# Optimization experiments

Measured on AMD Instinct MI355X. Metric: run time of the kernel, lower is better.

## Reference

```python
import jax, jax.numpy as jnp
import numpy as np

B, T, D = 4, 2048, 1024
E = 16            # routed experts
S = 2             # shared experts
MOE_TOPK = 2
COSINE_LAMBDA = 0.1


def setup_inputs() -> dict:
    key = jax.random.key(0)
    k_x, k_g, k_sh, k_rt = jax.random.split(key, 4)
    x = jax.random.normal(k_x, (B, T, D), dtype=jnp.float32)
    gate_w = jax.random.normal(k_g, (E, D), dtype=jnp.float32) * 0.02
    gate_b = jnp.zeros((E,), dtype=jnp.float32)
    shared_experts = jax.random.normal(k_sh, (S, D), dtype=jnp.float32) * 0.1
    routed_experts = jax.random.normal(k_rt, (E, D), dtype=jnp.float32) * 0.1
    return {"x": x, "gate_w": gate_w, "gate_b": gate_b,
            "shared_experts": shared_experts, "routed_experts": routed_experts}


def reference(x, gate_w, gate_b, shared_experts, routed_experts):
    b, t, d = x.shape
    n = b * t
    hidden = x.reshape(n, d)                                   # [N, D]

    # ---- router ----
    logits = hidden @ gate_w.T + gate_b                        # [N, E]
    probs = jax.nn.softmax(logits, axis=-1)                    # stable (shift-invariant)
    topk_vals, topk_idx = jax.lax.top_k(probs, MOE_TOPK)       # [N, K]
    if MOE_TOPK == 1:
        weights = jnp.ones_like(topk_vals)
    else:
        weights = topk_vals / jnp.clip(topk_vals.sum(-1, keepdims=True), 1e-6)

    # ---- shared experts (always active): sum_e hidden * w_e ----
    shared_sum = hidden * shared_experts.sum(0)                # [N, D]

    # ---- dense all-expert elementwise scale (as in original) ----
    routed_outs = hidden[None, :, :] * routed_experts[:, None, :]   # [E, N, D]

    # ---- diversity loss: cosine sim between flattened expert outputs ----
    flat = routed_outs.reshape(E, -1)                          # [E, N*D]
    norms = jnp.maximum(jnp.linalg.norm(flat, axis=1, keepdims=True), 1e-8)
    normed = flat / norms
    sim = jnp.clip(normed @ normed.T, -1.0, 1.0)               # [E, E]
    mask = 1.0 - jnp.eye(E, dtype=sim.dtype)
    div_loss = (sim * mask).sum() / max(E * (E - 1), 1) * COSINE_LAMBDA

    # ---- top-k gather + weighted combine ----
    routed_nd = routed_outs.transpose(1, 0, 2)                 # [N, E, D]
    sel = jnp.take_along_axis(routed_nd, topk_idx[:, :, None], axis=1)  # [N, K, D]
    dyn_sum = (sel * weights[:, :, None]).sum(axis=1)          # [N, D]

    out = (shared_sum + dyn_sum).reshape(b, t, d)
    return out, div_loss
```

## Files before the change

### kernel.cpp

```cpp
#include <hip/hip_runtime.h>

#define NTOK 8192
#define DDIM 1024
#define NEXP 16
#define NPAIR 136
#define NREP 8
#define XROW 1032

typedef float vfloat4 __attribute__((ext_vector_type(4)));

#define WS_GWT 0
#define WS_SG  16384
#define WS_GP  (16384 + NREP * DDIM)
#define WS_RT  (16384 + NREP * DDIM + 16 * NPAIR)

__global__ __launch_bounds__(256) void moe_prep(
    const float* __restrict__ gate_w,
    float* __restrict__ ws)
{
    const int gid = blockIdx.x * 256 + threadIdx.x;
    const int e = gid & 15;
    const int d4 = gid >> 4;
    const float4* gw4 = (const float4*)gate_w;
    float4* gwT4 = (float4*)(ws + WS_GWT);
    gwT4[d4 * 16 + e] = gw4[e * 256 + d4];
    float* s_glob = ws + WS_SG;
    s_glob[gid] = 0.f;
    s_glob[gid + 4096] = 0.f;
}

__global__ __launch_bounds__(256, 4) void moe_route(
    const float* __restrict__ x,
    const float* __restrict__ gate_b,
    float* __restrict__ ws)
{
    __shared__ float xt[8][XROW];

    const int t = threadIdx.x;
    const int b = blockIdx.x;
    const float4* gwT4 = (const float4*)(ws + WS_GWT);
    float* s_glob = ws + WS_SG;
    float4* route = (float4*)(ws + WS_RT);

    float4 ss = make_float4(0.f, 0.f, 0.f, 0.f);
    {
        const float4* x4 = (const float4*)x + (size_t)b * 2048;
        #pragma unroll
        for (int i = 0; i < 8; ++i) {
            float4 v = x4[i * 256 + t];
            *(float4*)&xt[i][4 * t] = v;
            ss.x = fmaf(v.x, v.x, ss.x);
            ss.y = fmaf(v.y, v.y, ss.y);
            ss.z = fmaf(v.z, v.z, ss.z);
            ss.w = fmaf(v.w, v.w, ss.w);
        }
    }
    __syncthreads();

    const int lane = t & 63;
    const int wave = t >> 6;
    const int e = lane & 15;
    const int h = (lane >> 4) & 1;
    const int g = lane >> 5;

    const int tokL = wave * 2 + g;
    const float* xrow = &xt[tokL][h * 512];
    const float4* gt = gwT4 + h * 128 * 16;
    float4 a4 = make_float4(0.f, 0.f, 0.f, 0.f);
    #pragma unroll 8
    for (int i = 0; i < 128; ++i) {
        float4 xv = *(const float4*)(xrow + 4 * i);
        float4 gv = gt[i * 16 + e];
        a4.x = fmaf(xv.x, gv.x, a4.x);
        a4.y = fmaf(xv.y, gv.y, a4.y);
        a4.z = fmaf(xv.z, gv.z, a4.z);
        a4.w = fmaf(xv.w, gv.w, a4.w);
    }
    float acc = (a4.x + a4.y) + (a4.z + a4.w);
    acc += __shfl_xor(acc, 16, 64);
    acc += gate_b[e];

    float v0 = -3.0e38f, v1 = -3.0e38f;
    int i0 = 0, i1 = 0;
    const int base = lane & 32;
    #pragma unroll
    for (int j = 0; j < NEXP; ++j) {
        float lv = __shfl(acc, base + j, 64);
        if (lv > v0)      { v1 = v0; i1 = i0; v0 = lv; i0 = j; }
        else if (lv > v1) { v1 = lv; i1 = j; }
    }
    float ex = __expf(v1 - v0);
    float w0 = 1.f / (1.f + ex);
    float w1 = ex * w0;

    if ((lane & 31) == 0)
        route[b * 8 + tokL] =
            make_float4(w0, w1, __int_as_float(i0), __int_as_float(i1));

    {
        float* rep = s_glob + (size_t)(b & (NREP - 1)) * DDIM;
        atomicAdd(&rep[4 * t + 0], ss.x);
        atomicAdd(&rep[4 * t + 1], ss.y);
        atomicAdd(&rep[4 * t + 2], ss.z);
        atomicAdd(&rep[4 * t + 3], ss.w);
    }
}

__global__ __launch_bounds__(256, 8) void moe_combine(
    const float* __restrict__ x,
    const float* __restrict__ sh,
    const float* __restrict__ re,
    const float* __restrict__ ws,
    float* __restrict__ out)
{
    const int t = threadIdx.x;
    const int lane = t & 63;
    const int n = blockIdx.x * 4 + (t >> 6);
    const float4* route = (const float4*)(ws + WS_RT);

    float4 rec = route[n];
    const float a0 = rec.x, a1 = rec.y;
    const int e0 = __float_as_int(rec.z);
    const int e1 = __float_as_int(rec.w);

    const float4* s0 = (const float4*)sh;
    const float4* s1 = (const float4*)(sh + DDIM);
    const float4* xr = (const float4*)(x + (size_t)n * DDIM);
    const float4* r0 = (const float4*)(re + (size_t)e0 * DDIM);
    const float4* r1 = (const float4*)(re + (size_t)e1 * DDIM);
    vfloat4* o = (vfloat4*)(out + (size_t)n * DDIM);

    #pragma unroll
    for (int j = 0; j < 4; ++j) {
        const int idx = lane + 64 * j;
        float4 xv = xr[idx];
        float4 p  = s0[idx];
        float4 q  = s1[idx];
        float4 b0 = r0[idx];
        float4 b1 = r1[idx];
        vfloat4 r;
        r.x = xv.x * ((p.x + q.x) + a0 * b0.x + a1 * b1.x);
        r.y = xv.y * ((p.y + q.y) + a0 * b0.y + a1 * b1.y);
        r.z = xv.z * ((p.z + q.z) + a0 * b0.z + a1 * b1.z);
        r.w = xv.w * ((p.w + q.w) + a0 * b0.w + a1 * b1.w);
        __builtin_nontemporal_store(r, &o[idx]);
    }
}

__global__ __launch_bounds__(320) void moe_div_partial(
    const float* __restrict__ re,
    float* __restrict__ ws)
{
    __shared__ float reT[64][17];
    __shared__ float s4[4][64];
    __shared__ float s_loc[64];

    const int t = threadIdx.x;
    const int b = blockIdx.x;
    const int d0 = b * 64;
    const float* s_glob = ws + WS_SG;
    float* G_part = ws + WS_GP;

    if (t < 256) {
        int c = t & 63, r = t >> 6;
        s4[r][c] = s_glob[r * DDIM + d0 + c] + s_glob[(r + 4) * DDIM + d0 + c];
        int e = t >> 4, d4 = t & 15;
        float4 v = ((const float4*)(re + (size_t)e * DDIM + d0))[d4];
        reT[d4 * 4 + 0][e] = v.x;
        reT[d4 * 4 + 1][e] = v.y;
        reT[d4 * 4 + 2][e] = v.z;
        reT[d4 * 4 + 3][e] = v.w;
    }
    __syncthreads();
    if (t < 64) s_loc[t] = (s4[0][t] + s4[1][t]) + (s4[2][t] + s4[3][t]);
    __syncthreads();

    const int p = t >> 1;
    const int half = t & 1;
    float a = 0.f;
    if (p < NPAIR) {
        int pe = 0, rem = p;
        while (rem >= NEXP - pe) { rem -= NEXP - pe; ++pe; }
        int pf = pe + rem;
        #pragma unroll
        for (int i = 0; i < 32; ++i) {
            int dd = half * 32 + i;
            a += s_loc[dd] * reT[dd][pe] * reT[dd][pf];
        }
    }
    a += __shfl_down(a, 1, 64);
    if (p < NPAIR && half == 0) G_part[b * NPAIR + p] = a;
}

__global__ __launch_bounds__(192) void moe_div_final(
    const float* __restrict__ ws,
    float* __restrict__ div_out)
{
    __shared__ float G[NPAIR];
    __shared__ float nr[NEXP];
    __shared__ float lsum;
    const float* G_part = ws + WS_GP;
    const int t = threadIdx.x;

    if (t == 0) lsum = 0.f;
    if (t < NPAIR) {
        float g = 0.f;
        #pragma unroll
        for (int b = 0; b < 16; ++b) g += G_part[b * NPAIR + t];
        G[t] = g;
    }
    __syncthreads();
    if (t < NEXP) {
        int idx = t * NEXP - (t * (t - 1)) / 2;
        nr[t] = fmaxf(sqrtf(G[idx]), 1e-8f);
    }
    __syncthreads();
    if (t < NPAIR) {
        int pe = 0, rem = t;
        while (rem >= NEXP - pe) { rem -= NEXP - pe; ++pe; }
        int pf = pe + rem;
        if (pe != pf) {
            float sim = G[t] / (nr[pe] * nr[pf]);
            sim = fminf(1.f, fmaxf(-1.f, sim));
            atomicAdd(&lsum, 2.f * sim);
        }
    }
    __syncthreads();
    if (t == 0) *div_out = lsum / (float)(NEXP * (NEXP - 1)) * 0.1f;
}

extern "C" void kernel_launch(void* const* d_in, const int* in_sizes, int n_in,
                              void* d_out, int out_size, void* d_ws, size_t ws_size,
                              hipStream_t stream) {
    const float* x  = (const float*)d_in[0];
    const float* gw = (const float*)d_in[1];
    const float* gb = (const float*)d_in[2];
    const float* sh = (const float*)d_in[3];
    const float* re = (const float*)d_in[4];
    float* out = (float*)d_out;
    float* ws = (float*)d_ws;

    moe_prep<<<16, 256, 0, stream>>>(gw, ws);
    moe_route<<<1024, 256, 0, stream>>>(x, gb, ws);
    moe_combine<<<2048, 256, 0, stream>>>(x, sh, re, ws, out);
    moe_div_partial<<<16, 320, 0, stream>>>(re, ws);
    moe_div_final<<<1, 192, 0, stream>>>(ws, out + (size_t)NTOK * DDIM);
}
```

Before: 154.5 us.

## Fuse router and combine kernels so x is read once from LDS

Merges the routing kernel and the combine kernel into one kernel. Each block handles 4 tokens: it stages x in shared memory, computes gate logits with the transposed gate weights streamed through LDS in chunks, picks the top-2, and writes the output directly from the staged x. This removes the second global read of x and the route buffer round trip. It also doubles the sum-of-squares replica count to spread atomic contention. It drops the nontemporal store, and the chunked gate loop adds extra block syncs per token group.

```diff
diff --git a/kernel.cpp b/kernel.cpp
--- a/kernel.cpp
+++ b/kernel.cpp
@@ -4,15 +4,13 @@
 #define DDIM 1024
 #define NEXP 16
 #define NPAIR 136
-#define NREP 8
-#define XROW 1032
-
-typedef float vfloat4 __attribute__((ext_vector_type(4)));
+#define NREP 16
+#define NCHUNK 8
+#define CK 128
 
 #define WS_GWT 0
 #define WS_SG  16384
 #define WS_GP  (16384 + NREP * DDIM)
-#define WS_RT  (16384 + NREP * DDIM + 16 * NPAIR)
 
 __global__ __launch_bounds__(256) void moe_prep(
     const float* __restrict__ gate_w,
@@ -25,28 +23,32 @@
     float4* gwT4 = (float4*)(ws + WS_GWT);
     gwT4[d4 * 16 + e] = gw4[e * 256 + d4];
     float* s_glob = ws + WS_SG;
-    s_glob[gid] = 0.f;
-    s_glob[gid + 4096] = 0.f;
-}
-
-__global__ __launch_bounds__(256, 4) void moe_route(
+    s_glob[gid]         = 0.f;
+    s_glob[gid + 4096]  = 0.f;
+    s_glob[gid + 8192]  = 0.f;
+    s_glob[gid + 12288] = 0.f;
+}
+
+__global__ __launch_bounds__(256, 6) void moe_fused(
     const float* __restrict__ x,
     const float* __restrict__ gate_b,
+    const float* __restrict__ sh,
+    const float* __restrict__ re,
+    float* __restrict__ out,
     float* __restrict__ ws)
 {
-    __shared__ float xt[8][XROW];
+    __shared__ float xt[4][DDIM];
+    __shared__ float4 gl[(CK / 4) * NEXP];
 
     const int t = threadIdx.x;
     const int b = blockIdx.x;
     const float4* gwT4 = (const float4*)(ws + WS_GWT);
-    float* s_glob = ws + WS_SG;
-    float4* route = (float4*)(ws + WS_RT);
 
     float4 ss = make_float4(0.f, 0.f, 0.f, 0.f);
     {
-        const float4* x4 = (const float4*)x + (size_t)b * 2048;
-        #pragma unroll
-        for (int i = 0; i < 8; ++i) {
+        const float4* x4 = (const float4*)x + (size_t)b * 1024;
+        #pragma unroll
+        for (int i = 0; i < 4; ++i) {
             float4 v = x4[i * 256 + t];
             *(float4*)&xt[i][4 * t] = v;
             ss.x = fmaf(v.x, v.x, ss.x);
@@ -58,34 +60,39 @@
     __syncthreads();
 
     const int lane = t & 63;
-    const int wave = t >> 6;
+    const int w = t >> 6;
     const int e = lane & 15;
-    const int h = (lane >> 4) & 1;
-    const int g = lane >> 5;
-
-    const int tokL = wave * 2 + g;
-    const float* xrow = &xt[tokL][h * 512];
-    const float4* gt = gwT4 + h * 128 * 16;
-    float4 a4 = make_float4(0.f, 0.f, 0.f, 0.f);
-    #pragma unroll 8
-    for (int i = 0; i < 128; ++i) {
-        float4 xv = *(const float4*)(xrow + 4 * i);
-        float4 gv = gt[i * 16 + e];
-        a4.x = fmaf(xv.x, gv.x, a4.x);
-        a4.y = fmaf(xv.y, gv.y, a4.y);
-        a4.z = fmaf(xv.z, gv.z, a4.z);
-        a4.w = fmaf(xv.w, gv.w, a4.w);
-    }
-    float acc = (a4.x + a4.y) + (a4.z + a4.w);
-    acc += __shfl_xor(acc, 16, 64);
-    acc += gate_b[e];
+    const int q = lane >> 4;
+
+    float4 acc = make_float4(0.f, 0.f, 0.f, 0.f);
+    for (int c = 0; c < NCHUNK; ++c) {
+        gl[t]       = gwT4[c * 512 + t];
+        gl[t + 256] = gwT4[c * 512 + 256 + t];
+        __syncthreads();
+        const float* xrow = &xt[w][c * CK];
+        #pragma unroll
+        for (int i = 0; i < 8; ++i) {
+            const int k4 = q * 8 + i;
+            float4 xv = *(const float4*)(xrow + 4 * k4);
+            float4 gv = gl[k4 * 16 + e];
+            acc.x = fmaf(xv.x, gv.x, acc.x);
+            acc.y = fmaf(xv.y, gv.y, acc.y);
+            acc.z = fmaf(xv.z, gv.z, acc.z);
+            acc.w = fmaf(xv.w, gv.w, acc.w);
+        }
+        __syncthreads();
+    }
+    float s = (acc.x + acc.y) + (acc.z + acc.w);
+    s += __shfl_xor(s, 16, 64);
+    s += __shfl_xor(s, 32, 64);
+    s += gate_b[e];
 
     float v0 = -3.0e38f, v1 = -3.0e38f;
     int i0 = 0, i1 = 0;
-    const int base = lane & 32;
+    const int base = lane & 48;
     #pragma unroll
     for (int j = 0; j < NEXP; ++j) {
-        float lv = __shfl(acc, base + j, 64);
+        float lv = __shfl(s, base + j, 64);
         if (lv > v0)      { v1 = v0; i1 = i0; v0 = lv; i0 = j; }
         else if (lv > v1) { v1 = lv; i1 = j; }
     }
@@ -93,57 +100,33 @@
     float w0 = 1.f / (1.f + ex);
     float w1 = ex * w0;
 
-    if ((lane & 31) == 0)
-        route[b * 8 + tokL] =
-            make_float4(w0, w1, __int_as_float(i0), __int_as_float(i1));
+    const float4* s0 = (const float4*)sh;
+    const float4* s1 = (const float4*)(sh + DDIM);
+    const float4* r0 = (const float4*)(re + (size_t)i0 * DDIM);
+    const float4* r1 = (const float4*)(re + (size_t)i1 * DDIM);
+    float4* o = (float4*)(out + ((size_t)b * 4 + w) * DDIM);
+    #pragma unroll
+    for (int j = 0; j < 4; ++j) {
+        const int idx = lane + 64 * j;
+        float4 xv = *(const float4*)&xt[w][4 * idx];
+        float4 p  = s0[idx];
+        float4 qq = s1[idx];
+        float4 b0 = r0[idx];
+        float4 b1 = r1[idx];
+        float4 r;
+        r.x = xv.x * ((p.x + qq.x) + w0 * b0.x + w1 * b1.x);
+        r.y = xv.y * ((p.y + qq.y) + w0 * b0.y + w1 * b1.y);
+        r.z = xv.z * ((p.z + qq.z) + w0 * b0.z + w1 * b1.z);
+        r.w = xv.w * ((p.w + qq.w) + w0 * b0.w + w1 * b1.w);
+        o[idx] = r;
+    }
 
     {
-        float* rep = s_glob + (size_t)(b & (NREP - 1)) * DDIM;
+        float* rep = ws + WS_SG + (size_t)(b & (NREP - 1)) * DDIM;
         atomicAdd(&rep[4 * t + 0], ss.x);
         atomicAdd(&rep[4 * t + 1], ss.y);
         atomicAdd(&rep[4 * t + 2], ss.z);
         atomicAdd(&rep[4 * t + 3], ss.w);
-    }
-}
-
-__global__ __launch_bounds__(256, 8) void moe_combine(
-    const float* __restrict__ x,
-    const float* __restrict__ sh,
-    const float* __restrict__ re,
-    const float* __restrict__ ws,
-    float* __restrict__ out)
-{
-    const int t = threadIdx.x;
-    const int lane = t & 63;
-    const int n = blockIdx.x * 4 + (t >> 6);
-    const float4* route = (const float4*)(ws + WS_RT);
-
-    float4 rec = route[n];
-    const float a0 = rec.x, a1 = rec.y;
-    const int e0 = __float_as_int(rec.z);
-    const int e1 = __float_as_int(rec.w);
-
-    const float4* s0 = (const float4*)sh;
-    const float4* s1 = (const float4*)(sh + DDIM);
-    const float4* xr = (const float4*)(x + (size_t)n * DDIM);
-    const float4* r0 = (const float4*)(re + (size_t)e0 * DDIM);
-    const float4* r1 = (const float4*)(re + (size_t)e1 * DDIM);
-    vfloat4* o = (vfloat4*)(out + (size_t)n * DDIM);
-
-    #pragma unroll
-    for (int j = 0; j < 4; ++j) {
-        const int idx = lane + 64 * j;
-        float4 xv = xr[idx];
-        float4 p  = s0[idx];
-        float4 q  = s1[idx];
-        float4 b0 = r0[idx];
-        float4 b1 = r1[idx];
-        vfloat4 r;
-        r.x = xv.x * ((p.x + q.x) + a0 * b0.x + a1 * b1.x);
-        r.y = xv.y * ((p.y + q.y) + a0 * b0.y + a1 * b1.y);
-        r.z = xv.z * ((p.z + q.z) + a0 * b0.z + a1 * b1.z);
-        r.w = xv.w * ((p.w + q.w) + a0 * b0.w + a1 * b1.w);
-        __builtin_nontemporal_store(r, &o[idx]);
     }
 }
 
@@ -163,7 +146,8 @@
 
     if (t < 256) {
         int c = t & 63, r = t >> 6;
-        s4[r][c] = s_glob[r * DDIM + d0 + c] + s_glob[(r + 4) * DDIM + d0 + c];
+        s4[r][c] = (s_glob[r * DDIM + d0 + c] + s_glob[(r + 4) * DDIM + d0 + c])
+                 + (s_glob[(r + 8) * DDIM + d0 + c] + s_glob[(r + 12) * DDIM + d0 + c]);
         int e = t >> 4, d4 = t & 15;
         float4 v = ((const float4*)(re + (size_t)e * DDIM + d0))[d4];
         reT[d4 * 4 + 0][e] = v.x;
@@ -241,8 +225,7 @@
     float* ws = (float*)d_ws;
 
     moe_prep<<<16, 256, 0, stream>>>(gw, ws);
-    moe_route<<<1024, 256, 0, stream>>>(x, gb, ws);
-    moe_combine<<<2048, 256, 0, stream>>>(x, sh, re, ws, out);
+    moe_fused<<<2048, 256, 0, stream>>>(x, gb, sh, re, out, ws);
     moe_div_partial<<<16, 320, 0, stream>>>(re, ws);
     moe_div_final<<<1, 192, 0, stream>>>(ws, out + (size_t)NTOK * DDIM);
 }
```

After: 132.8 us. -14.0%, faster.

## Fuse routing and combine into one kernel, replace atomics with per-block partial reduction

Applied to the files above, without the earlier changes.

Merges the router and combine kernels so each block reuses the 8 token rows already staged in shared memory, avoiding a second 32MB read of x and the route buffer round trip. The per-dimension sum of squares for the diversity loss is written as per-block partials and reduced by a new kernel when workspace allows, falling back to a single atomic-accumulated array otherwise. The gate dot product gets two accumulators for more ILP. Occupancy bound drops to 2 blocks per CU, and the partial buffer adds 4MB of writes plus an extra launch.

```diff
diff --git a/kernel.cpp b/kernel.cpp
--- a/kernel.cpp
+++ b/kernel.cpp
@@ -4,15 +4,16 @@
 #define DDIM 1024
 #define NEXP 16
 #define NPAIR 136
-#define NREP 8
 #define XROW 1032
+#define NBLK 1024
 
 typedef float vfloat4 __attribute__((ext_vector_type(4)));
 
 #define WS_GWT 0
 #define WS_SG  16384
-#define WS_GP  (16384 + NREP * DDIM)
-#define WS_RT  (16384 + NREP * DDIM + 16 * NPAIR)
+#define WS_GP  (16384 + DDIM)
+#define WS_SRED (16384 + DDIM + 16 * NPAIR)
+#define WS_NEED_F (WS_SRED + NBLK * DDIM)
 
 __global__ __launch_bounds__(256) void moe_prep(
     const float* __restrict__ gate_w,
@@ -22,16 +23,17 @@
     const int e = gid & 15;
     const int d4 = gid >> 4;
     const float4* gw4 = (const float4*)gate_w;
-    float4* gwT4 = (float4*)(ws + WS_GWT);
-    gwT4[d4 * 16 + e] = gw4[e * 256 + d4];
-    float* s_glob = ws + WS_SG;
-    s_glob[gid] = 0.f;
-    s_glob[gid + 4096] = 0.f;
-}
-
-__global__ __launch_bounds__(256, 4) void moe_route(
+    ((float4*)(ws + WS_GWT))[d4 * 16 + e] = gw4[e * 256 + d4];
+    if (gid < DDIM) (ws + WS_SG)[gid] = 0.f;
+}
+
+template<bool SRED>
+__global__ __launch_bounds__(256, 2) void moe_fused(
     const float* __restrict__ x,
     const float* __restrict__ gate_b,
+    const float* __restrict__ sh,
+    const float* __restrict__ re,
+    float* __restrict__ out,
     float* __restrict__ ws)
 {
     __shared__ float xt[8][XROW];
@@ -39,8 +41,6 @@
     const int t = threadIdx.x;
     const int b = blockIdx.x;
     const float4* gwT4 = (const float4*)(ws + WS_GWT);
-    float* s_glob = ws + WS_SG;
-    float4* route = (float4*)(ws + WS_RT);
 
     float4 ss = make_float4(0.f, 0.f, 0.f, 0.f);
     {
@@ -55,6 +55,15 @@
             ss.w = fmaf(v.w, v.w, ss.w);
         }
     }
+    if (SRED) {
+        ((float4*)(ws + WS_SRED + (size_t)b * DDIM))[t] = ss;
+    } else {
+        float* sg = ws + WS_SG;
+        atomicAdd(&sg[4 * t + 0], ss.x);
+        atomicAdd(&sg[4 * t + 1], ss.y);
+        atomicAdd(&sg[4 * t + 2], ss.z);
+        atomicAdd(&sg[4 * t + 3], ss.w);
+    }
     __syncthreads();
 
     const int lane = t & 63;
@@ -62,30 +71,38 @@
     const int e = lane & 15;
     const int h = (lane >> 4) & 1;
     const int g = lane >> 5;
-
     const int tokL = wave * 2 + g;
+
     const float* xrow = &xt[tokL][h * 512];
-    const float4* gt = gwT4 + h * 128 * 16;
-    float4 a4 = make_float4(0.f, 0.f, 0.f, 0.f);
+    const float4* gt = gwT4 + h * 128 * 16 + e;
+    float4 acc0 = make_float4(0.f, 0.f, 0.f, 0.f);
+    float4 acc1 = make_float4(0.f, 0.f, 0.f, 0.f);
     #pragma unroll 8
-    for (int i = 0; i < 128; ++i) {
-        float4 xv = *(const float4*)(xrow + 4 * i);
-        float4 gv = gt[i * 16 + e];
-        a4.x = fmaf(xv.x, gv.x, a4.x);
-        a4.y = fmaf(xv.y, gv.y, a4.y);
-        a4.z = fmaf(xv.z, gv.z, a4.z);
-        a4.w = fmaf(xv.w, gv.w, a4.w);
-    }
-    float acc = (a4.x + a4.y) + (a4.z + a4.w);
-    acc += __shfl_xor(acc, 16, 64);
-    acc += gate_b[e];
+    for (int i = 0; i < 128; i += 2) {
+        float4 xv0 = *(const float4*)(xrow + 4 * i);
+        float4 gv0 = gt[i * 16];
+        float4 xv1 = *(const float4*)(xrow + 4 * i + 4);
+        float4 gv1 = gt[i * 16 + 16];
+        acc0.x = fmaf(xv0.x, gv0.x, acc0.x);
+        acc0.y = fmaf(xv0.y, gv0.y, acc0.y);
+        acc0.z = fmaf(xv0.z, gv0.z, acc0.z);
+        acc0.w = fmaf(xv0.w, gv0.w, acc0.w);
+        acc1.x = fmaf(xv1.x, gv1.x, acc1.x);
+        acc1.y = fmaf(xv1.y, gv1.y, acc1.y);
+        acc1.z = fmaf(xv1.z, gv1.z, acc1.z);
+        acc1.w = fmaf(xv1.w, gv1.w, acc1.w);
+    }
+    float s = ((acc0.x + acc0.y) + (acc0.z + acc0.w))
+            + ((acc1.x + acc1.y) + (acc1.z + acc1.w));
+    s += __shfl_xor(s, 16, 64);
+    s += gate_b[e];
 
     float v0 = -3.0e38f, v1 = -3.0e38f;
     int i0 = 0, i1 = 0;
     const int base = lane & 32;
     #pragma unroll
     for (int j = 0; j < NEXP; ++j) {
-        float lv = __shfl(acc, base + j, 64);
+        float lv = __shfl(s, base + j, 64);
         if (lv > v0)      { v1 = v0; i1 = i0; v0 = lv; i0 = j; }
         else if (lv > v1) { v1 = lv; i1 = j; }
     }
@@ -93,57 +110,56 @@
     float w0 = 1.f / (1.f + ex);
     float w1 = ex * w0;
 
-    if ((lane & 31) == 0)
-        route[b * 8 + tokL] =
-            make_float4(w0, w1, __int_as_float(i0), __int_as_float(i1));
-
-    {
-        float* rep = s_glob + (size_t)(b & (NREP - 1)) * DDIM;
-        atomicAdd(&rep[4 * t + 0], ss.x);
-        atomicAdd(&rep[4 * t + 1], ss.y);
-        atomicAdd(&rep[4 * t + 2], ss.z);
-        atomicAdd(&rep[4 * t + 3], ss.w);
-    }
-}
-
-__global__ __launch_bounds__(256, 8) void moe_combine(
-    const float* __restrict__ x,
-    const float* __restrict__ sh,
-    const float* __restrict__ re,
-    const float* __restrict__ ws,
-    float* __restrict__ out)
-{
-    const int t = threadIdx.x;
-    const int lane = t & 63;
-    const int n = blockIdx.x * 4 + (t >> 6);
-    const float4* route = (const float4*)(ws + WS_RT);
-
-    float4 rec = route[n];
-    const float a0 = rec.x, a1 = rec.y;
-    const int e0 = __float_as_int(rec.z);
-    const int e1 = __float_as_int(rec.w);
-
     const float4* s0 = (const float4*)sh;
     const float4* s1 = (const float4*)(sh + DDIM);
-    const float4* xr = (const float4*)(x + (size_t)n * DDIM);
-    const float4* r0 = (const float4*)(re + (size_t)e0 * DDIM);
-    const float4* r1 = (const float4*)(re + (size_t)e1 * DDIM);
-    vfloat4* o = (vfloat4*)(out + (size_t)n * DDIM);
-
     #pragma unroll
-    for (int j = 0; j < 4; ++j) {
-        const int idx = lane + 64 * j;
-        float4 xv = xr[idx];
-        float4 p  = s0[idx];
-        float4 q  = s1[idx];
-        float4 b0 = r0[idx];
-        float4 b1 = r1[idx];
-        vfloat4 r;
-        r.x = xv.x * ((p.x + q.x) + a0 * b0.x + a1 * b1.x);
-        r.y = xv.y * ((p.y + q.y) + a0 * b0.y + a1 * b1.y);
-        r.z = xv.z * ((p.z + q.z) + a0 * b0.z + a1 * b1.z);
-        r.w = xv.w * ((p.w + q.w) + a0 * b0.w + a1 * b1.w);
-        __builtin_nontemporal_store(r, &o[idx]);
+    for (int tk = 0; tk < 2; ++tk) {
+        const int src = tk << 5;
+        float a0 = __shfl(w0, src, 64);
+        float a1 = __shfl(w1, src, 64);
+        int   e0 = __shfl(i0, src, 64);
+        int   e1 = __shfl(i1, src, 64);
+        const int tokC = wave * 2 + tk;
+        const float4* xr = (const float4*)&xt[tokC][0];
+        const float4* r0 = (const float4*)(re + (size_t)e0 * DDIM);
+        const float4* r1 = (const float4*)(re + (size_t)e1 * DDIM);
+        vfloat4* o = (vfloat4*)(out + ((size_t)b * 8 + tokC) * DDIM);
+        #pragma unroll
+        for (int j = 0; j < 4; ++j) {
+            const int idx = lane + 64 * j;
+            float4 xv = xr[idx];
+            float4 p  = s0[idx];
+            float4 q  = s1[idx];
+            float4 b0 = r0[idx];
+            float4 b1 = r1[idx];
+            vfloat4 r;
+            r.x = xv.x * ((p.x + q.x) + a0 * b0.x + a1 * b1.x);
+            r.y = xv.y * ((p.y + q.y) + a0 * b0.y + a1 * b1.y);
+            r.z = xv.z * ((p.z + q.z) + a0 * b0.z + a1 * b1.z);
+            r.w = xv.w * ((p.w + q.w) + a0 * b0.w + a1 * b1.w);
+            __builtin_nontemporal_store(r, &o[idx]);
+        }
+    }
+}
+
+__global__ __launch_bounds__(256) void moe_sreduce(
+    float* __restrict__ ws)
+{
+    __shared__ float part[8][33];
+    const int t = threadIdx.x;
+    const int d0 = blockIdx.x * 32;
+    const int c = t & 31;
+    const int rg = t >> 5;
+    const float* sred = ws + WS_SRED;
+    float a = 0.f;
+    for (int r = rg; r < NBLK; r += 8)
+        a += sred[(size_t)r * DDIM + d0 + c];
+    part[rg][c] = a;
+    __syncthreads();
+    if (t < 32) {
+        float v = ((part[0][t] + part[1][t]) + (part[2][t] + part[3][t]))
+                + ((part[4][t] + part[5][t]) + (part[6][t] + part[7][t]));
+        (ws + WS_SG)[d0 + t] = v;
     }
 }
 
@@ -152,18 +168,15 @@
     float* __restrict__ ws)
 {
     __shared__ float reT[64][17];
-    __shared__ float s4[4][64];
     __shared__ float s_loc[64];
 
     const int t = threadIdx.x;
     const int b = blockIdx.x;
     const int d0 = b * 64;
-    const float* s_glob = ws + WS_SG;
     float* G_part = ws + WS_GP;
 
+    if (t < 64) s_loc[t] = (ws + WS_SG)[d0 + t];
     if (t < 256) {
-        int c = t & 63, r = t >> 6;
-        s4[r][c] = s_glob[r * DDIM + d0 + c] + s_glob[(r + 4) * DDIM + d0 + c];
         int e = t >> 4, d4 = t & 15;
         float4 v = ((const float4*)(re + (size_t)e * DDIM + d0))[d4];
         reT[d4 * 4 + 0][e] = v.x;
@@ -171,8 +184,6 @@
         reT[d4 * 4 + 2][e] = v.z;
         reT[d4 * 4 + 3][e] = v.w;
     }
-    __syncthreads();
-    if (t < 64) s_loc[t] = (s4[0][t] + s4[1][t]) + (s4[2][t] + s4[3][t]);
     __syncthreads();
 
     const int p = t >> 1;
@@ -240,9 +251,15 @@
     float* out = (float*)d_out;
     float* ws = (float*)d_ws;
 
+    const bool sred = ws_size >= (size_t)WS_NEED_F * sizeof(float);
+
     moe_prep<<<16, 256, 0, stream>>>(gw, ws);
-    moe_route<<<1024, 256, 0, stream>>>(x, gb, ws);
-    moe_combine<<<2048, 256, 0, stream>>>(x, sh, re, ws, out);
+    if (sred) {
+        moe_fused<true><<<NBLK, 256, 0, stream>>>(x, gb, sh, re, out, ws);
+        moe_sreduce<<<32, 256, 0, stream>>>(ws);
+    } else {
+        moe_fused<false><<<NBLK, 256, 0, stream>>>(x, gb, sh, re, out, ws);
+    }
     moe_div_partial<<<16, 320, 0, stream>>>(re, ws);
     moe_div_final<<<1, 192, 0, stream>>>(ws, out + (size_t)NTOK * DDIM);
 }
```

New measurement: 158.6 us. 2.7% more time.
